# Performance work log

Hardware: AMD Instinct MI355X
Metric: run time of the kernel (lower is better)

Reference implementation:

```python
import jax, jax.numpy as jnp
import numpy as np

B, N, F_IN, F_E = 8, 64, 32, 16   # batch, nodes, node feat, edge feat
H = 64    # hidden_state_size
M = 64    # message_size
EH = 50   # edge_hidden_dim
T = 12    # l_target
RD = 200  # readout hidden_dim
NL = 3    # n_layers (message passing iterations, weight-tied)


def setup_inputs() -> dict:
    key = jax.random.key(0)
    ks = jax.random.split(key, 16)
    s = 0.05
    return {
        "g": jax.random.uniform(ks[0], (B, N, N), dtype=jnp.float32),
        "h_in": jax.random.uniform(ks[1], (B, N, F_IN), dtype=jnp.float32),
        "e": jax.random.normal(ks[2], (B, N, N, F_E), dtype=jnp.float32),
        # edge network MLP: edge_feat -> EH -> M*H
        "We1": jax.random.normal(ks[3], (F_E, EH)) * s,
        "be1": jnp.zeros((EH,)),
        "We2": jax.random.normal(ks[4], (EH, M * H)) * s,
        "be2": jnp.zeros((M * H,)),
        # GRU update (input = message M, hidden = H); gate order r, z, n
        "W_ih": jax.random.normal(ks[5], (3 * H, M)) * s,
        "W_hh": jax.random.normal(ks[6], (3 * H, H)) * s,
        "b_ih": jnp.zeros((3 * H,)),
        "b_hh": jnp.zeros((3 * H,)),
        # readout i-net: [h_T, h_0] (2H) -> RD -> T ; j-net: h_T (H) -> RD -> T
        "Wi1": jax.random.normal(ks[7], (2 * H, RD)) * s,
        "bi1": jnp.zeros((RD,)),
        "Wi2": jax.random.normal(ks[8], (RD, T)) * s,
        "bi2": jnp.zeros((T,)),
        "Wj1": jax.random.normal(ks[9], (H, RD)) * s,
        "bj1": jnp.zeros((RD,)),
        "Wj2": jax.random.normal(ks[10], (RD, T)) * s,
        "bj2": jnp.zeros((T,)),
    }


def reference(g, h_in, e, We1, be1, We2, be2, W_ih, W_hh, b_ih, b_hh,
              Wi1, bi1, Wi2, bi2, Wj1, bj1, Wj2, bj2):
    dt = h_in.dtype
    # pad node features with zeros up to hidden_state_size H
    h0 = jnp.concatenate(
        [h_in, jnp.zeros(h_in.shape[:2] + (H - F_IN,), dt)], axis=-1)  # (B,N,H)
    node_valid = (jnp.sum(h_in, axis=2) > 0).astype(dt)  # (B,N) mask applied each layer

    # edge network: per-edge (M,H) matrix A(e_vw); depends only on e, so compute once
    A = jnp.maximum(e @ We1 + be1, 0.0) @ We2 + be2        # (B,N,N,M*H)
    A = A.reshape(B, N, N, M, H)

    h = h0
    for _ in range(NL):
        # m[b,j] = sum_i g[b,i,j] * A(e[b,i,j]) @ h[b,i]
        # (original materializes m as (B,N,N,M), multiplies by g, sums over dim 1)
        m = jnp.einsum('bij,bijmh,bih->bjm', g, A, h)       # (B,N,M)
        # GRU cell update (PyTorch gate order: r, z, n)
        gi = m @ W_ih.T + b_ih                              # (B,N,3H)
        gh = h @ W_hh.T + b_hh
        r = jax.nn.sigmoid(gi[..., :H] + gh[..., :H])
        z = jax.nn.sigmoid(gi[..., H:2 * H] + gh[..., H:2 * H])
        n = jnp.tanh(gi[..., 2 * H:] + r * gh[..., 2 * H:])
        h = (1.0 - z) * n + z * h
        # zero out padding nodes: (sum(h_in,2) > 0) * h_t
        h = node_valid[..., None] * h

    # readout: R = sum_v mask_v * sigmoid(i([h_v^T, h_v^0])) * j(h_v^T)
    cat = jnp.concatenate([h, h0], axis=-1)                 # (B,N,2H)
    i_act = jax.nn.sigmoid(jnp.maximum(cat @ Wi1 + bi1, 0.0) @ Wi2 + bi2)
    j_act = jnp.maximum(h @ Wj1 + bj1, 0.0) @ Wj2 + bj2
    res = jnp.sum(node_valid[..., None] * i_act * j_act, axis=1)  # (B,T)
    return res
```

## Files before the change

### kernel.cpp

```cpp
#include <hip/hip_runtime.h>
#include <math.h>

#define BB 8
#define NN 64
#define F_IN 32
#define F_E 16
#define HH 64
#define MM 64
#define EHD 50
#define TT 12
#define RD 200
#define NL 3

#define KP 52
#define WROWS (KP * MM)
#define RLEN (NN * KP)
#define NODES (BB * NN)
#define IG 32

#define OFF_WAUG  0
#define SZ_WAUG   (WROWS * HH)
#define OFF_H0    (OFF_WAUG + SZ_WAUG)
#define OFF_H     (OFF_H0 + NODES * HH)
#define OFF_VALID (OFF_H + NODES * HH)
#define OFF_UG    (OFF_VALID + NODES)
#define SZ_UG     (BB * NN * RLEN)
#define OFF_C     (OFF_UG + SZ_UG)
#define SZ_C      (NODES * WROWS)
#define OFF_MPART (OFF_C + SZ_C)
#define SZ_MPART  (BB * IG * NN * MM)

__global__ __launch_bounds__(256) void prep_kernel(const float* __restrict__ h_in,
                                                   const float* __restrict__ We2,
                                                   const float* __restrict__ be2,
                                                   float* __restrict__ ws,
                                                   float* __restrict__ out) {
    int idx = blockIdx.x * 256 + threadIdx.x;
    float* Waug  = ws + OFF_WAUG;
    float* h0    = ws + OFF_H0;
    float* h     = ws + OFF_H;
    float* valid = ws + OFF_VALID;
    if (idx < SZ_WAUG) {
        int km = idx >> 6;
        int hv = idx & 63;
        int k  = km >> 6;
        int m  = km & 63;
        float v = 0.0f;
        if (k < EHD)       v = We2[k * (MM * HH) + m * HH + hv];
        else if (k == EHD) v = be2[m * HH + hv];
        Waug[idx] = v;
    } else if (idx < SZ_WAUG + NODES * HH) {
        int t = idx - SZ_WAUG;
        int n = t >> 6;
        int hv = t & 63;
        float v = (hv < F_IN) ? h_in[n * F_IN + hv] : 0.0f;
        h0[t] = v;
        h[t]  = v;
    } else if (idx < SZ_WAUG + NODES * HH + NODES) {
        int n = idx - SZ_WAUG - NODES * HH;
        float s = 0.0f;
        for (int c = 0; c < F_IN; ++c) s += h_in[n * F_IN + c];
        valid[n] = (s > 0.0f) ? 1.0f : 0.0f;
    } else if (idx < SZ_WAUG + NODES * HH + NODES + BB * TT) {
        out[idx - (SZ_WAUG + NODES * HH + NODES)] = 0.0f;
    }
}

__global__ __launch_bounds__(256) void edge_kernel(const float* __restrict__ g,
                                                   const float* __restrict__ e,
                                                   const float* __restrict__ We1,
                                                   const float* __restrict__ be1,
                                                   float* __restrict__ ws) {
    __shared__ float w1[F_E * EHD];
    __shared__ float b1[EHD];
    for (int t = threadIdx.x; t < F_E * EHD; t += 256) w1[t] = We1[t];
    if (threadIdx.x < EHD) b1[threadIdx.x] = be1[threadIdx.x];
    __syncthreads();

    int idx = blockIdx.x * 256 + threadIdx.x;
    int i = idx & 63;
    int j = (idx >> 6) & 63;
    int b = idx >> 12;

    const float* ep = e + ((size_t)((b * NN + i) * NN + j)) * F_E;
    float ev[F_E];
#pragma unroll
    for (int c = 0; c < F_E; c += 4) {
        float4 v = *(const float4*)(ep + c);
        ev[c] = v.x; ev[c + 1] = v.y; ev[c + 2] = v.z; ev[c + 3] = v.w;
    }
    float gv = g[(b * NN + i) * NN + j];

    float acc[EHD];
#pragma unroll
    for (int k = 0; k < EHD; ++k) acc[k] = b1[k];
#pragma unroll
    for (int c = 0; c < F_E; ++c) {
        float evc = ev[c];
#pragma unroll
        for (int k = 0; k < EHD; ++k) acc[k] += evc * w1[c * EHD + k];
    }
    float* ugp = ws + OFF_UG + ((size_t)(b * NN + j) * NN + i) * KP;
#pragma unroll
    for (int k = 0; k < EHD; ++k) ugp[k] = gv * fmaxf(acc[k], 0.0f);
    ugp[EHD]     = gv;
    ugp[EHD + 1] = 0.0f;
}

#define CG_BM 32
#define CG_BN 128
__global__ __launch_bounds__(256) void cgemm_kernel(float* __restrict__ ws) {
    const float* h    = ws + OFF_H;
    const float* Waug = ws + OFF_WAUG;
    float* C          = ws + OFF_C;

    __shared__ float hs[CG_BM * HH];
    __shared__ float wsh[CG_BN * HH];

    int tid = threadIdx.x;
    int kt = blockIdx.x;
    int nt = blockIdx.y;

    {
        const float4* src = (const float4*)(h + nt * CG_BM * HH);
        float4* dst = (float4*)hs;
#pragma unroll
        for (int q = 0; q < 2; ++q) dst[tid + q * 256] = src[tid + q * 256];
    }
    {
        const float4* src = (const float4*)(Waug + (size_t)kt * CG_BN * HH);
        float4* dst = (float4*)wsh;
#pragma unroll
        for (int q = 0; q < 8; ++q) {
            int fi = tid + q * 256;
            int row = fi >> 4, slot = fi & 15;
            dst[(row << 4) | (slot ^ (row & 15))] = src[fi];
        }
    }
    __syncthreads();

    int cg = tid & 31;
    int rg = tid >> 5;
    float acc[4][4];
#pragma unroll
    for (int q = 0; q < 4; ++q)
#pragma unroll
        for (int p = 0; p < 4; ++p) acc[q][p] = 0.0f;

#pragma unroll
    for (int hv = 0; hv < HH; hv += 4) {
        int slot = hv >> 2;
        float4 a[4], w[4];
#pragma unroll
        for (int q = 0; q < 4; ++q)
            a[q] = *(const float4*)(hs + (rg * 4 + q) * HH + hv);
#pragma unroll
        for (int p = 0; p < 4; ++p) {
            int row = cg + 32 * p;
            w[p] = ((const float4*)wsh)[(row << 4) | (slot ^ (row & 15))];
        }
#pragma unroll
        for (int q = 0; q < 4; ++q)
#pragma unroll
            for (int p = 0; p < 4; ++p)
                acc[q][p] += a[q].x * w[p].x + a[q].y * w[p].y +
                             a[q].z * w[p].z + a[q].w * w[p].w;
    }

#pragma unroll
    for (int q = 0; q < 4; ++q) {
        int node = nt * CG_BM + rg * 4 + q;
#pragma unroll
        for (int p = 0; p < 4; ++p) {
            int km = kt * CG_BN + cg + 32 * p;
            C[(size_t)node * WROWS + km] = acc[q][p];
        }
    }
}

__global__ __launch_bounds__(256) void msg_tiled_kernel(float* __restrict__ ws) {
    int blk = blockIdx.x;
    int b   = blk >> 5;
    int ig  = blk & 31;
    int i0  = ig * 2;

    const float* Cg  = ws + OFF_C  + (size_t)(b * NN + i0) * WROWS;
    const float* ugg = ws + OFF_UG + (size_t)(b * NN) * RLEN + i0 * KP;
    float* mp = ws + OFF_MPART + (size_t)(b * IG + ig) * (NN * MM);

    __shared__ float ug_t[104][64];
    __shared__ float C_s[104 * 64];

    int tid = threadIdx.x;
    {
        const float4* src = (const float4*)Cg;
        float4* dst = (float4*)C_s;
        for (int f = tid; f < 1664; f += 256) dst[f] = src[f];
    }
    {
        for (int f = tid; f < 1664; f += 256) {
            int j = f / 26, kq = f - j * 26;
            float4 v = *(const float4*)(ugg + (size_t)j * RLEN + kq * 4);
            ug_t[kq * 4 + 0][j] = v.x;
            ug_t[kq * 4 + 1][j] = v.y;
            ug_t[kq * 4 + 2][j] = v.z;
            ug_t[kq * 4 + 3][j] = v.w;
        }
    }
    __syncthreads();

    int tx = tid & 15;
    int ty = tid >> 4;
    float acc[4][4];
#pragma unroll
    for (int q = 0; q < 4; ++q)
#pragma unroll
        for (int p = 0; p < 4; ++p) acc[q][p] = 0.0f;

    const float4* C4 = (const float4*)C_s;
#pragma unroll 4
    for (int k = 0; k < 104; ++k) {
        float4 bv = C4[k * 16 + tx];
        float4 av = *(const float4*)(&ug_t[k][ty * 4]);
        acc[0][0] += av.x * bv.x; acc[0][1] += av.x * bv.y; acc[0][2] += av.x * bv.z; acc[0][3] += av.x * bv.w;
        acc[1][0] += av.y * bv.x; acc[1][1] += av.y * bv.y; acc[1][2] += av.y * bv.z; acc[1][3] += av.y * bv.w;
        acc[2][0] += av.z * bv.x; acc[2][1] += av.z * bv.y; acc[2][2] += av.z * bv.z; acc[2][3] += av.z * bv.w;
        acc[3][0] += av.w * bv.x; acc[3][1] += av.w * bv.y; acc[3][2] += av.w * bv.z; acc[3][3] += av.w * bv.w;
    }

#pragma unroll
    for (int q = 0; q < 4; ++q) {
        float4 o; o.x = acc[q][0]; o.y = acc[q][1]; o.z = acc[q][2]; o.w = acc[q][3];
        *(float4*)(mp + (size_t)(ty * 4 + q) * MM + tx * 4) = o;
    }
}

__global__ __launch_bounds__(256) void gru_reduce_kernel(const float* __restrict__ W_ih,
                                                         const float* __restrict__ W_hh,
                                                         const float* __restrict__ b_ih,
                                                         const float* __restrict__ b_hh,
                                                         float* __restrict__ ws) {
    int bj = blockIdx.x;
    int b = bj >> 6;
    int j = bj & 63;

    const float* mpart_g = ws + OFF_MPART;
    float* h           = ws + OFF_H;
    const float* valid = ws + OFF_VALID;

    __shared__ float mpart[4][MM];
    __shared__ float mv[MM];
    __shared__ float hv[HH];
    __shared__ float gi_s[3 * HH], gh_s[3 * HH];

    int lane = threadIdx.x & 63;
    int w    = threadIdx.x >> 6;

    if (threadIdx.x < HH) hv[threadIdx.x] = h[(size_t)bj * HH + threadIdx.x];

    float s = 0.0f;
#pragma unroll
    for (int q = 0; q < 8; ++q) {
        int ig = w * 8 + q;
        s += mpart_g[((size_t)(b * IG + ig) * NN + j) * MM + lane];
    }
    mpart[w][lane] = s;
    __syncthreads();

    if (threadIdx.x < MM)
        mv[threadIdx.x] = mpart[0][threadIdx.x] + mpart[1][threadIdx.x] +
                          mpart[2][threadIdx.x] + mpart[3][threadIdx.x];
    __syncthreads();

    if (threadIdx.x < 3 * HH) {
        int x = threadIdx.x;
        float gi = b_ih[x], gh = b_hh[x];
        const float4* wi = (const float4*)(W_ih + x * MM);
        const float4* wh = (const float4*)(W_hh + x * HH);
#pragma unroll
        for (int c = 0; c < HH / 4; ++c) {
            float4 aw = wi[c], bw = wh[c];
            gi += aw.x * mv[c * 4] + aw.y * mv[c * 4 + 1] + aw.z * mv[c * 4 + 2] + aw.w * mv[c * 4 + 3];
            gh += bw.x * hv[c * 4] + bw.y * hv[c * 4 + 1] + bw.z * hv[c * 4 + 2] + bw.w * hv[c * 4 + 3];
        }
        gi_s[x] = gi;
        gh_s[x] = gh;
    }
    __syncthreads();

    if (threadIdx.x < HH) {
        int t = threadIdx.x;
        float r = 1.0f / (1.0f + expf(-(gi_s[t] + gh_s[t])));
        float z = 1.0f / (1.0f + expf(-(gi_s[HH + t] + gh_s[HH + t])));
        float n = tanhf(gi_s[2 * HH + t] + r * gh_s[2 * HH + t]);
        float hn = (1.0f - z) * n + z * hv[t];
        h[(size_t)bj * HH + t] = hn * valid[bj];
    }
}

__global__ __launch_bounds__(64) void readout_kernel(const float* __restrict__ Wi1,
                                                     const float* __restrict__ bi1,
                                                     const float* __restrict__ Wi2,
                                                     const float* __restrict__ bi2,
                                                     const float* __restrict__ Wj1,
                                                     const float* __restrict__ bj1,
                                                     const float* __restrict__ Wj2,
                                                     const float* __restrict__ bj2,
                                                     float* __restrict__ ws,
                                                     float* __restrict__ out) {
    int node = blockIdx.x;
    int b = node >> 6;
    int t = threadIdx.x;

    __shared__ float cat[2 * HH];
    __shared__ float ih[RD], jh[RD];

    const float* h  = ws + OFF_H;
    const float* h0 = ws + OFF_H0;
    const float* valid = ws + OFF_VALID;

    cat[t]      = h[(size_t)node * HH + t];
    cat[64 + t] = h0[(size_t)node * HH + t];
    __syncthreads();

    bool has3 = (t + 192 < RD);
    int u3 = has3 ? (t + 192) : 0;
    float a0 = bi1[t], a1 = bi1[t + 64], a2 = bi1[t + 128], a3 = has3 ? bi1[u3] : 0.f;
    for (int c = 0; c < 2 * HH; ++c) {
        float cv = cat[c];
        const float* wr = Wi1 + c * RD;
        a0 += cv * wr[t];
        a1 += cv * wr[t + 64];
        a2 += cv * wr[t + 128];
        a3 += cv * wr[u3];
    }
    ih[t] = fmaxf(a0, 0.f); ih[t + 64] = fmaxf(a1, 0.f); ih[t + 128] = fmaxf(a2, 0.f);
    if (has3) ih[u3] = fmaxf(a3, 0.f);

    float c0 = bj1[t], c1 = bj1[t + 64], c2 = bj1[t + 128], c3 = has3 ? bj1[u3] : 0.f;
    for (int c = 0; c < HH; ++c) {
        float hvv = cat[c];
        const float* wr = Wj1 + c * RD;
        c0 += hvv * wr[t];
        c1 += hvv * wr[t + 64];
        c2 += hvv * wr[t + 128];
        c3 += hvv * wr[u3];
    }
    jh[t] = fmaxf(c0, 0.f); jh[t + 64] = fmaxf(c1, 0.f); jh[t + 128] = fmaxf(c2, 0.f);
    if (has3) jh[u3] = fmaxf(c3, 0.f);
    __syncthreads();

    if (t < TT) {
        float i2 = bi2[t], j2 = bj2[t];
        for (int u = 0; u < RD; ++u) {
            i2 += ih[u] * Wi2[u * TT + t];
            j2 += jh[u] * Wj2[u * TT + t];
        }
        float sig = 1.0f / (1.0f + expf(-i2));
        float contrib = valid[node] * sig * j2;
        atomicAdd(&out[b * TT + t], contrib);
    }
}

extern "C" void kernel_launch(void* const* d_in, const int* in_sizes, int n_in,
                              void* d_out, int out_size, void* d_ws, size_t ws_size,
                              hipStream_t stream) {
    (void)in_sizes; (void)n_in; (void)out_size; (void)ws_size;
    const float* g    = (const float*)d_in[0];
    const float* h_in = (const float*)d_in[1];
    const float* e    = (const float*)d_in[2];
    const float* We1  = (const float*)d_in[3];
    const float* be1  = (const float*)d_in[4];
    const float* We2  = (const float*)d_in[5];
    const float* be2  = (const float*)d_in[6];
    const float* W_ih = (const float*)d_in[7];
    const float* W_hh = (const float*)d_in[8];
    const float* b_ih = (const float*)d_in[9];
    const float* b_hh = (const float*)d_in[10];
    const float* Wi1  = (const float*)d_in[11];
    const float* bi1  = (const float*)d_in[12];
    const float* Wi2  = (const float*)d_in[13];
    const float* bi2  = (const float*)d_in[14];
    const float* Wj1  = (const float*)d_in[15];
    const float* bj1  = (const float*)d_in[16];
    const float* Wj2  = (const float*)d_in[17];
    const float* bj2  = (const float*)d_in[18];
    float* out = (float*)d_out;
    float* ws  = (float*)d_ws;

    const int prep_elems = SZ_WAUG + NODES * HH + NODES + BB * TT;
    prep_kernel<<<(prep_elems + 255) / 256, 256, 0, stream>>>(h_in, We2, be2, ws, out);
    edge_kernel<<<(BB * NN * NN) / 256, 256, 0, stream>>>(g, e, We1, be1, ws);

    for (int l = 0; l < NL; ++l) {
        cgemm_kernel<<<dim3(WROWS / CG_BN, NODES / CG_BM), 256, 0, stream>>>(ws);
        msg_tiled_kernel<<<BB * IG, 256, 0, stream>>>(ws);
        gru_reduce_kernel<<<NODES, 256, 0, stream>>>(W_ih, W_hh, b_ih, b_hh, ws);
    }

    readout_kernel<<<NODES, 64, 0, stream>>>(Wi1, bi1, Wi2, bi2, Wj1, bj1, Wj2, bj2, ws, out);
}
```

Measured before the change: 214.7 us.

## Fuse all stages into one cooperative persistent kernel with grid syncs

Replaces the eleven separate kernel launches (prep, edge, and cgemm/msg/gru per layer, readout) with a single cooperative kernel of 256 blocks that runs every stage and uses grid.sync between stages. The message kernel now stages one source node at a time to use less shared memory, and readout runs on 256-thread blocks. The goal is to remove per-launch overhead and tail gaps between the many small kernels. In exchange, grid-wide barriers add cost, fewer blocks cover the cgemm and GRU work, and the prep stage runs on only 128 blocks; a fallback multi-kernel path is kept in case the cooperative launch fails.

Measured after the change: 839.6 us. +291.0%, slower.

```diff
diff --git a/kernel.cpp b/kernel.cpp
--- a/kernel.cpp
+++ b/kernel.cpp
@@ -1,5 +1,8 @@
 #include <hip/hip_runtime.h>
+#include <hip/hip_cooperative_groups.h>
 #include <math.h>
+
+namespace cg = cooperative_groups;
 
 #define BB 8
 #define NN 64
@@ -18,69 +21,64 @@
 #define NODES (BB * NN)
 #define IG 32
 
+#define NTHR 256
+#define NBLK 256
+
 #define OFF_WAUG  0
 #define SZ_WAUG   (WROWS * HH)
 #define OFF_H0    (OFF_WAUG + SZ_WAUG)
 #define OFF_H     (OFF_H0 + NODES * HH)
 #define OFF_VALID (OFF_H + NODES * HH)
 #define OFF_UG    (OFF_VALID + NODES)
-#define SZ_UG     (BB * NN * RLEN)
+#define SZ_UG     (NODES * RLEN)
 #define OFF_C     (OFF_UG + SZ_UG)
 #define SZ_C      (NODES * WROWS)
 #define OFF_MPART (OFF_C + SZ_C)
 #define SZ_MPART  (BB * IG * NN * MM)
 
-__global__ __launch_bounds__(256) void prep_kernel(const float* __restrict__ h_in,
-                                                   const float* __restrict__ We2,
-                                                   const float* __restrict__ be2,
-                                                   float* __restrict__ ws,
-                                                   float* __restrict__ out) {
-    int idx = blockIdx.x * 256 + threadIdx.x;
+#define PREP_ELEMS (SZ_WAUG + NODES * HH + NODES + BB * TT)
+
+__device__ __forceinline__ void do_prep(int idx0, int stride,
+    const float* __restrict__ h_in, const float* __restrict__ We2,
+    const float* __restrict__ be2, float* __restrict__ ws, float* __restrict__ out)
+{
     float* Waug  = ws + OFF_WAUG;
     float* h0    = ws + OFF_H0;
     float* h     = ws + OFF_H;
     float* valid = ws + OFF_VALID;
-    if (idx < SZ_WAUG) {
-        int km = idx >> 6;
-        int hv = idx & 63;
-        int k  = km >> 6;
-        int m  = km & 63;
-        float v = 0.0f;
-        if (k < EHD)       v = We2[k * (MM * HH) + m * HH + hv];
-        else if (k == EHD) v = be2[m * HH + hv];
-        Waug[idx] = v;
-    } else if (idx < SZ_WAUG + NODES * HH) {
-        int t = idx - SZ_WAUG;
-        int n = t >> 6;
-        int hv = t & 63;
-        float v = (hv < F_IN) ? h_in[n * F_IN + hv] : 0.0f;
-        h0[t] = v;
-        h[t]  = v;
-    } else if (idx < SZ_WAUG + NODES * HH + NODES) {
-        int n = idx - SZ_WAUG - NODES * HH;
-        float s = 0.0f;
-        for (int c = 0; c < F_IN; ++c) s += h_in[n * F_IN + c];
-        valid[n] = (s > 0.0f) ? 1.0f : 0.0f;
-    } else if (idx < SZ_WAUG + NODES * HH + NODES + BB * TT) {
-        out[idx - (SZ_WAUG + NODES * HH + NODES)] = 0.0f;
-    }
-}
-
-__global__ __launch_bounds__(256) void edge_kernel(const float* __restrict__ g,
-                                                   const float* __restrict__ e,
-                                                   const float* __restrict__ We1,
-                                                   const float* __restrict__ be1,
-                                                   float* __restrict__ ws) {
-    __shared__ float w1[F_E * EHD];
-    __shared__ float b1[EHD];
-    for (int t = threadIdx.x; t < F_E * EHD; t += 256) w1[t] = We1[t];
-    if (threadIdx.x < EHD) b1[threadIdx.x] = be1[threadIdx.x];
-    __syncthreads();
-
-    int idx = blockIdx.x * 256 + threadIdx.x;
-    int i = idx & 63;
-    int j = (idx >> 6) & 63;
-    int b = idx >> 12;
+    for (int idx = idx0; idx < PREP_ELEMS; idx += stride) {
+        if (idx < SZ_WAUG) {
+            int km = idx >> 6, hv = idx & 63;
+            int k = km >> 6, m = km & 63;
+            float v = 0.0f;
+            if (k < EHD)       v = We2[k * (MM * HH) + m * HH + hv];
+            else if (k == EHD) v = be2[m * HH + hv];
+            Waug[idx] = v;
+        } else if (idx < SZ_WAUG + NODES * HH) {
+            int t = idx - SZ_WAUG;
+            int n = t >> 6, hv = t & 63;
+            float v = (hv < F_IN) ? h_in[n * F_IN + hv] : 0.0f;
+            h0[t] = v;
+            h[t]  = v;
+        } else if (idx < SZ_WAUG + NODES * HH + NODES) {
+            int n = idx - SZ_WAUG - NODES * HH;
+            float s = 0.0f;
+            for (int c = 0; c < F_IN; ++c) s += h_in[n * F_IN + c];
+            valid[n] = (s > 0.0f) ? 1.0f : 0.0f;
+        } else {
+            out[idx - (SZ_WAUG + NODES * HH + NODES)] = 0.0f;
+        }
+    }
+}
+
+__device__ __forceinline__ void do_edge(int eid,
+    const float* __restrict__ g, const float* __restrict__ e,
+    const float* __restrict__ w1, const float* __restrict__ b1,
+    float* __restrict__ ws)
+{
+    int i = eid & 63;
+    int j = (eid >> 6) & 63;
+    int b = eid >> 12;
 
     const float* ep = e + ((size_t)((b * NN + i) * NN + j)) * F_E;
     float ev[F_E];
@@ -107,28 +105,23 @@
     ugp[EHD + 1] = 0.0f;
 }
 
-#define CG_BM 32
-#define CG_BN 128
-__global__ __launch_bounds__(256) void cgemm_kernel(float* __restrict__ ws) {
+__device__ __forceinline__ void do_cgemm_tile(int kt, int nt, int tid,
+    float* __restrict__ lds, float* __restrict__ ws)
+{
     const float* h    = ws + OFF_H;
     const float* Waug = ws + OFF_WAUG;
     float* C          = ws + OFF_C;
-
-    __shared__ float hs[CG_BM * HH];
-    __shared__ float wsh[CG_BN * HH];
-
-    int tid = threadIdx.x;
-    int kt = blockIdx.x;
-    int nt = blockIdx.y;
+    float* hs  = lds;
+    float* wsh = lds + 2048;
 
     {
-        const float4* src = (const float4*)(h + nt * CG_BM * HH);
+        const float4* src = (const float4*)(h + nt * 32 * HH);
         float4* dst = (float4*)hs;
 #pragma unroll
         for (int q = 0; q < 2; ++q) dst[tid + q * 256] = src[tid + q * 256];
     }
     {
-        const float4* src = (const float4*)(Waug + (size_t)kt * CG_BN * HH);
+        const float4* src = (const float4*)(Waug + (size_t)kt * 128 * HH);
         float4* dst = (float4*)wsh;
 #pragma unroll
         for (int q = 0; q < 8; ++q) {
@@ -139,8 +132,8 @@
     }
     __syncthreads();
 
-    int cg = tid & 31;
-    int rg = tid >> 5;
+    int cgl = tid & 31;
+    int rg  = tid >> 5;
     float acc[4][4];
 #pragma unroll
     for (int q = 0; q < 4; ++q)
@@ -156,7 +149,7 @@
             a[q] = *(const float4*)(hs + (rg * 4 + q) * HH + hv);
 #pragma unroll
         for (int p = 0; p < 4; ++p) {
-            int row = cg + 32 * p;
+            int row = cgl + 32 * p;
             w[p] = ((const float4*)wsh)[(row << 4) | (slot ^ (row & 15))];
         }
 #pragma unroll
@@ -166,48 +159,24 @@
                 acc[q][p] += a[q].x * w[p].x + a[q].y * w[p].y +
                              a[q].z * w[p].z + a[q].w * w[p].w;
     }
+    __syncthreads();
 
 #pragma unroll
     for (int q = 0; q < 4; ++q) {
-        int node = nt * CG_BM + rg * 4 + q;
+        int node = nt * 32 + rg * 4 + q;
 #pragma unroll
         for (int p = 0; p < 4; ++p) {
-            int km = kt * CG_BN + cg + 32 * p;
+            int km = kt * 128 + cgl + 32 * p;
             C[(size_t)node * WROWS + km] = acc[q][p];
         }
     }
 }
 
-__global__ __launch_bounds__(256) void msg_tiled_kernel(float* __restrict__ ws) {
-    int blk = blockIdx.x;
-    int b   = blk >> 5;
-    int ig  = blk & 31;
-    int i0  = ig * 2;
-
-    const float* Cg  = ws + OFF_C  + (size_t)(b * NN + i0) * WROWS;
-    const float* ugg = ws + OFF_UG + (size_t)(b * NN) * RLEN + i0 * KP;
-    float* mp = ws + OFF_MPART + (size_t)(b * IG + ig) * (NN * MM);
-
-    __shared__ float ug_t[104][64];
-    __shared__ float C_s[104 * 64];
-
-    int tid = threadIdx.x;
-    {
-        const float4* src = (const float4*)Cg;
-        float4* dst = (float4*)C_s;
-        for (int f = tid; f < 1664; f += 256) dst[f] = src[f];
-    }
-    {
-        for (int f = tid; f < 1664; f += 256) {
-            int j = f / 26, kq = f - j * 26;
-            float4 v = *(const float4*)(ugg + (size_t)j * RLEN + kq * 4);
-            ug_t[kq * 4 + 0][j] = v.x;
-            ug_t[kq * 4 + 1][j] = v.y;
-            ug_t[kq * 4 + 2][j] = v.z;
-            ug_t[kq * 4 + 3][j] = v.w;
-        }
-    }
-    __syncthreads();
+__device__ __forceinline__ void do_msg_pair(int b, int ig, int tid,
+    float* __restrict__ lds, float* __restrict__ ws)
+{
+    float* C_s  = lds;
+    float* ug_t = lds + 3328;
 
     int tx = tid & 15;
     int ty = tid >> 4;
@@ -217,17 +186,39 @@
 #pragma unroll
         for (int p = 0; p < 4; ++p) acc[q][p] = 0.0f;
 
-    const float4* C4 = (const float4*)C_s;
+    for (int ii = 0; ii < 2; ++ii) {
+        int i = ig * 2 + ii;
+        const float* Cg  = ws + OFF_C  + (size_t)(b * NN + i) * WROWS;
+        const float* ugg = ws + OFF_UG + (size_t)(b * NN) * RLEN + i * KP;
+        {
+            const float4* src = (const float4*)Cg;
+            float4* dst = (float4*)C_s;
+            for (int f = tid; f < 832; f += NTHR) dst[f] = src[f];
+        }
+        for (int f = tid; f < 832; f += NTHR) {
+            int j = f / 13, kq = f - j * 13;
+            float4 v = *(const float4*)(ugg + (size_t)j * RLEN + kq * 4);
+            ug_t[(kq * 4 + 0) * 64 + j] = v.x;
+            ug_t[(kq * 4 + 1) * 64 + j] = v.y;
+            ug_t[(kq * 4 + 2) * 64 + j] = v.z;
+            ug_t[(kq * 4 + 3) * 64 + j] = v.w;
+        }
+        __syncthreads();
+
+        const float4* C4 = (const float4*)C_s;
 #pragma unroll 4
-    for (int k = 0; k < 104; ++k) {
-        float4 bv = C4[k * 16 + tx];
-        float4 av = *(const float4*)(&ug_t[k][ty * 4]);
-        acc[0][0] += av.x * bv.x; acc[0][1] += av.x * bv.y; acc[0][2] += av.x * bv.z; acc[0][3] += av.x * bv.w;
-        acc[1][0] += av.y * bv.x; acc[1][1] += av.y * bv.y; acc[1][2] += av.y * bv.z; acc[1][3] += av.y * bv.w;
-        acc[2][0] += av.z * bv.x; acc[2][1] += av.z * bv.y; acc[2][2] += av.z * bv.z; acc[2][3] += av.z * bv.w;
-        acc[3][0] += av.w * bv.x; acc[3][1] += av.w * bv.y; acc[3][2] += av.w * bv.z; acc[3][3] += av.w * bv.w;
-    }
-
+        for (int k = 0; k < KP; ++k) {
+            float4 bv = C4[k * 16 + tx];
+            float4 av = *(const float4*)(ug_t + k * 64 + ty * 4);
+            acc[0][0] += av.x * bv.x; acc[0][1] += av.x * bv.y; acc[0][2] += av.x * bv.z; acc[0][3] += av.x * bv.w;
+            acc[1][0] += av.y * bv.x; acc[1][1] += av.y * bv.y; acc[1][2] += av.y * bv.z; acc[1][3] += av.y * bv.w;
+            acc[2][0] += av.z * bv.x; acc[2][1] += av.z * bv.y; acc[2][2] += av.z * bv.z; acc[2][3] += av.z * bv.w;
+            acc[3][0] += av.w * bv.x; acc[3][1] += av.w * bv.y; acc[3][2] += av.w * bv.z; acc[3][3] += av.w * bv.w;
+        }
+        __syncthreads();
+    }
+
+    float* mp = ws + OFF_MPART + (size_t)(b * IG + ig) * (NN * MM);
 #pragma unroll
     for (int q = 0; q < 4; ++q) {
         float4 o; o.x = acc[q][0]; o.y = acc[q][1]; o.z = acc[q][2]; o.w = acc[q][3];
@@ -235,45 +226,38 @@
     }
 }
 
-__global__ __launch_bounds__(256) void gru_reduce_kernel(const float* __restrict__ W_ih,
-                                                         const float* __restrict__ W_hh,
-                                                         const float* __restrict__ b_ih,
-                                                         const float* __restrict__ b_hh,
-                                                         float* __restrict__ ws) {
-    int bj = blockIdx.x;
-    int b = bj >> 6;
-    int j = bj & 63;
-
-    const float* mpart_g = ws + OFF_MPART;
+__device__ __forceinline__ void do_gru(int node, int tid,
+    float* __restrict__ lds, float* __restrict__ ws,
+    const float* __restrict__ W_ih, const float* __restrict__ W_hh,
+    const float* __restrict__ b_ih, const float* __restrict__ b_hh)
+{
+    int b = node >> 6, j = node & 63;
+    float* mpart = lds;
+    float* mv    = lds + 256;
+    float* hvs   = lds + 320;
+    float* gi_s  = lds + 384;
+    float* gh_s  = lds + 576;
     float* h           = ws + OFF_H;
     const float* valid = ws + OFF_VALID;
 
-    __shared__ float mpart[4][MM];
-    __shared__ float mv[MM];
-    __shared__ float hv[HH];
-    __shared__ float gi_s[3 * HH], gh_s[3 * HH];
-
-    int lane = threadIdx.x & 63;
-    int w    = threadIdx.x >> 6;
-
-    if (threadIdx.x < HH) hv[threadIdx.x] = h[(size_t)bj * HH + threadIdx.x];
+    int lane = tid & 63, w = tid >> 6;
+    if (tid < HH) hvs[tid] = h[(size_t)node * HH + tid];
 
     float s = 0.0f;
 #pragma unroll
     for (int q = 0; q < 8; ++q) {
         int ig = w * 8 + q;
-        s += mpart_g[((size_t)(b * IG + ig) * NN + j) * MM + lane];
-    }
-    mpart[w][lane] = s;
-    __syncthreads();
-
-    if (threadIdx.x < MM)
-        mv[threadIdx.x] = mpart[0][threadIdx.x] + mpart[1][threadIdx.x] +
-                          mpart[2][threadIdx.x] + mpart[3][threadIdx.x];
-    __syncthreads();
-
-    if (threadIdx.x < 3 * HH) {
-        int x = threadIdx.x;
+        s += ws[OFF_MPART + ((size_t)(b * IG + ig) * NN + j) * MM + lane];
+    }
+    mpart[w * 64 + lane] = s;
+    __syncthreads();
+
+    if (tid < MM)
+        mv[tid] = mpart[tid] + mpart[64 + tid] + mpart[128 + tid] + mpart[192 + tid];
+    __syncthreads();
+
+    if (tid < 3 * HH) {
+        int x = tid;
         float gi = b_ih[x], gh = b_hh[x];
         const float4* wi = (const float4*)(W_ih + x * MM);
         const float4* wh = (const float4*)(W_hh + x * HH);
@@ -281,85 +265,164 @@
         for (int c = 0; c < HH / 4; ++c) {
             float4 aw = wi[c], bw = wh[c];
             gi += aw.x * mv[c * 4] + aw.y * mv[c * 4 + 1] + aw.z * mv[c * 4 + 2] + aw.w * mv[c * 4 + 3];
-            gh += bw.x * hv[c * 4] + bw.y * hv[c * 4 + 1] + bw.z * hv[c * 4 + 2] + bw.w * hv[c * 4 + 3];
+            gh += bw.x * hvs[c * 4] + bw.y * hvs[c * 4 + 1] + bw.z * hvs[c * 4 + 2] + bw.w * hvs[c * 4 + 3];
         }
         gi_s[x] = gi;
         gh_s[x] = gh;
     }
     __syncthreads();
 
-    if (threadIdx.x < HH) {
-        int t = threadIdx.x;
-        float r = 1.0f / (1.0f + expf(-(gi_s[t] + gh_s[t])));
-        float z = 1.0f / (1.0f + expf(-(gi_s[HH + t] + gh_s[HH + t])));
-        float n = tanhf(gi_s[2 * HH + t] + r * gh_s[2 * HH + t]);
-        float hn = (1.0f - z) * n + z * hv[t];
-        h[(size_t)bj * HH + t] = hn * valid[bj];
-    }
-}
-
-__global__ __launch_bounds__(64) void readout_kernel(const float* __restrict__ Wi1,
-                                                     const float* __restrict__ bi1,
-                                                     const float* __restrict__ Wi2,
-                                                     const float* __restrict__ bi2,
-                                                     const float* __restrict__ Wj1,
-                                                     const float* __restrict__ bj1,
-                                                     const float* __restrict__ Wj2,
-                                                     const float* __restrict__ bj2,
-                                                     float* __restrict__ ws,
-                                                     float* __restrict__ out) {
-    int node = blockIdx.x;
+    if (tid < HH) {
+        float r = 1.0f / (1.0f + expf(-(gi_s[tid] + gh_s[tid])));
+        float z = 1.0f / (1.0f + expf(-(gi_s[HH + tid] + gh_s[HH + tid])));
+        float n = tanhf(gi_s[2 * HH + tid] + r * gh_s[2 * HH + tid]);
+        float hn = (1.0f - z) * n + z * hvs[tid];
+        h[(size_t)node * HH + tid] = hn * valid[node];
+    }
+    __syncthreads();
+}
+
+__device__ __forceinline__ void do_readout(int node, int tid,
+    float* __restrict__ lds, float* __restrict__ ws,
+    const float* __restrict__ Wi1, const float* __restrict__ bi1,
+    const float* __restrict__ Wi2, const float* __restrict__ bi2,
+    const float* __restrict__ Wj1, const float* __restrict__ bj1,
+    const float* __restrict__ Wj2, const float* __restrict__ bj2,
+    float* __restrict__ out)
+{
+    float* cat = lds;
+    float* ih  = lds + 128;
+    float* jh  = lds + 328;
+    const float* h     = ws + OFF_H;
+    const float* h0    = ws + OFF_H0;
+    const float* valid = ws + OFF_VALID;
     int b = node >> 6;
-    int t = threadIdx.x;
-
-    __shared__ float cat[2 * HH];
-    __shared__ float ih[RD], jh[RD];
-
-    const float* h  = ws + OFF_H;
-    const float* h0 = ws + OFF_H0;
-    const float* valid = ws + OFF_VALID;
-
-    cat[t]      = h[(size_t)node * HH + t];
-    cat[64 + t] = h0[(size_t)node * HH + t];
-    __syncthreads();
-
-    bool has3 = (t + 192 < RD);
-    int u3 = has3 ? (t + 192) : 0;
-    float a0 = bi1[t], a1 = bi1[t + 64], a2 = bi1[t + 128], a3 = has3 ? bi1[u3] : 0.f;
-    for (int c = 0; c < 2 * HH; ++c) {
-        float cv = cat[c];
-        const float* wr = Wi1 + c * RD;
-        a0 += cv * wr[t];
-        a1 += cv * wr[t + 64];
-        a2 += cv * wr[t + 128];
-        a3 += cv * wr[u3];
-    }
-    ih[t] = fmaxf(a0, 0.f); ih[t + 64] = fmaxf(a1, 0.f); ih[t + 128] = fmaxf(a2, 0.f);
-    if (has3) ih[u3] = fmaxf(a3, 0.f);
-
-    float c0 = bj1[t], c1 = bj1[t + 64], c2 = bj1[t + 128], c3 = has3 ? bj1[u3] : 0.f;
-    for (int c = 0; c < HH; ++c) {
-        float hvv = cat[c];
-        const float* wr = Wj1 + c * RD;
-        c0 += hvv * wr[t];
-        c1 += hvv * wr[t + 64];
-        c2 += hvv * wr[t + 128];
-        c3 += hvv * wr[u3];
-    }
-    jh[t] = fmaxf(c0, 0.f); jh[t + 64] = fmaxf(c1, 0.f); jh[t + 128] = fmaxf(c2, 0.f);
-    if (has3) jh[u3] = fmaxf(c3, 0.f);
-    __syncthreads();
-
-    if (t < TT) {
-        float i2 = bi2[t], j2 = bj2[t];
+
+    if (tid < 2 * HH)
+        cat[tid] = (tid < HH) ? h[(size_t)node * HH + tid]
+                              : h0[(size_t)node * HH + (tid - HH)];
+    __syncthreads();
+
+    if (tid < RD) {
+        float a = bi1[tid];
+        for (int c = 0; c < 2 * HH; ++c) a += cat[c] * Wi1[c * RD + tid];
+        ih[tid] = fmaxf(a, 0.0f);
+        float bj = bj1[tid];
+        for (int c = 0; c < HH; ++c) bj += cat[c] * Wj1[c * RD + tid];
+        jh[tid] = fmaxf(bj, 0.0f);
+    }
+    __syncthreads();
+
+    if (tid < TT) {
+        float i2 = bi2[tid], j2 = bj2[tid];
         for (int u = 0; u < RD; ++u) {
-            i2 += ih[u] * Wi2[u * TT + t];
-            j2 += jh[u] * Wj2[u * TT + t];
+            i2 += ih[u] * Wi2[u * TT + tid];
+            j2 += jh[u] * Wj2[u * TT + tid];
         }
         float sig = 1.0f / (1.0f + expf(-i2));
-        float contrib = valid[node] * sig * j2;
-        atomicAdd(&out[b * TT + t], contrib);
-    }
+        atomicAdd(&out[b * TT + tid], valid[node] * sig * j2);
+    }
+    __syncthreads();
+}
+
+__global__ __launch_bounds__(NTHR) void mega_kernel(
+    const float* __restrict__ g,   const float* __restrict__ h_in,
+    const float* __restrict__ e,
+    const float* __restrict__ We1, const float* __restrict__ be1,
+    const float* __restrict__ We2, const float* __restrict__ be2,
+    const float* __restrict__ W_ih, const float* __restrict__ W_hh,
+    const float* __restrict__ b_ih, const float* __restrict__ b_hh,
+    const float* __restrict__ Wi1, const float* __restrict__ bi1,
+    const float* __restrict__ Wi2, const float* __restrict__ bi2,
+    const float* __restrict__ Wj1, const float* __restrict__ bj1,
+    const float* __restrict__ Wj2, const float* __restrict__ bj2,
+    float* __restrict__ ws, float* __restrict__ out)
+{
+    cg::grid_group grid = cg::this_grid();
+    __shared__ float lds[10240];
+
+    const int blk = blockIdx.x;
+    const int tid = threadIdx.x;
+
+    if (blk < 128) {
+        do_prep(blk * NTHR + tid, 128 * NTHR, h_in, We2, be2, ws, out);
+    } else {
+        float* w1 = lds;
+        float* b1 = lds + F_E * EHD;
+        for (int t = tid; t < F_E * EHD; t += NTHR) w1[t] = We1[t];
+        if (tid < EHD) b1[tid] = be1[tid];
+        __syncthreads();
+        do_edge((blk - 128) * NTHR + tid, g, e, w1, b1, ws);
+    }
+    __threadfence(); grid.sync();
+
+    for (int l = 0; l < NL; ++l) {
+        for (int t = blk; t < 416; t += NBLK)
+            do_cgemm_tile(t % 26, t / 26, tid, lds, ws);
+        __threadfence(); grid.sync();
+
+        do_msg_pair(blk >> 5, blk & 31, tid, lds, ws);
+        __threadfence(); grid.sync();
+
+        for (int n = blk; n < NODES; n += NBLK)
+            do_gru(n, tid, lds, ws, W_ih, W_hh, b_ih, b_hh);
+        __threadfence(); grid.sync();
+    }
+
+    for (int n = blk; n < NODES; n += NBLK)
+        do_readout(n, tid, lds, ws, Wi1, bi1, Wi2, bi2, Wj1, bj1, Wj2, bj2, out);
+}
+
+__global__ __launch_bounds__(NTHR) void k_prep(const float* __restrict__ h_in,
+    const float* __restrict__ We2, const float* __restrict__ be2,
+    float* __restrict__ ws, float* __restrict__ out)
+{
+    do_prep(blockIdx.x * NTHR + threadIdx.x, gridDim.x * NTHR, h_in, We2, be2, ws, out);
+}
+
+__global__ __launch_bounds__(NTHR) void k_edge(const float* __restrict__ g,
+    const float* __restrict__ e, const float* __restrict__ We1,
+    const float* __restrict__ be1, float* __restrict__ ws)
+{
+    __shared__ float lds[F_E * EHD + EHD];
+    float* w1 = lds;
+    float* b1 = lds + F_E * EHD;
+    for (int t = threadIdx.x; t < F_E * EHD; t += NTHR) w1[t] = We1[t];
+    if (threadIdx.x < EHD) b1[threadIdx.x] = be1[threadIdx.x];
+    __syncthreads();
+    do_edge(blockIdx.x * NTHR + threadIdx.x, g, e, w1, b1, ws);
+}
+
+__global__ __launch_bounds__(NTHR) void k_cgemm(float* __restrict__ ws)
+{
+    __shared__ float lds[10240];
+    do_cgemm_tile(blockIdx.x % 26, blockIdx.x / 26, threadIdx.x, lds, ws);
+}
+
+__global__ __launch_bounds__(NTHR) void k_msg(float* __restrict__ ws)
+{
+    __shared__ float lds[6656];
+    do_msg_pair(blockIdx.x >> 5, blockIdx.x & 31, threadIdx.x, lds, ws);
+}
+
+__global__ __launch_bounds__(NTHR) void k_gru(const float* __restrict__ W_ih,
+    const float* __restrict__ W_hh, const float* __restrict__ b_ih,
+    const float* __restrict__ b_hh, float* __restrict__ ws)
+{
+    __shared__ float lds[768];
+    do_gru(blockIdx.x, threadIdx.x, lds, ws, W_ih, W_hh, b_ih, b_hh);
+}
+
+__global__ __launch_bounds__(NTHR) void k_readout(
+    const float* __restrict__ Wi1, const float* __restrict__ bi1,
+    const float* __restrict__ Wi2, const float* __restrict__ bi2,
+    const float* __restrict__ Wj1, const float* __restrict__ bj1,
+    const float* __restrict__ Wj2, const float* __restrict__ bj2,
+    float* __restrict__ ws, float* __restrict__ out)
+{
+    __shared__ float lds[528];
+    do_readout(blockIdx.x, threadIdx.x, lds, ws,
+               Wi1, bi1, Wi2, bi2, Wj1, bj1, Wj2, bj2, out);
 }
 
 extern "C" void kernel_launch(void* const* d_in, const int* in_sizes, int n_in,
@@ -388,15 +451,25 @@
     float* out = (float*)d_out;
     float* ws  = (float*)d_ws;
 
-    const int prep_elems = SZ_WAUG + NODES * HH + NODES + BB * TT;
-    prep_kernel<<<(prep_elems + 255) / 256, 256, 0, stream>>>(h_in, We2, be2, ws, out);
-    edge_kernel<<<(BB * NN * NN) / 256, 256, 0, stream>>>(g, e, We1, be1, ws);
-
-    for (int l = 0; l < NL; ++l) {
-        cgemm_kernel<<<dim3(WROWS / CG_BN, NODES / CG_BM), 256, 0, stream>>>(ws);
-        msg_tiled_kernel<<<BB * IG, 256, 0, stream>>>(ws);
-        gru_reduce_kernel<<<NODES, 256, 0, stream>>>(W_ih, W_hh, b_ih, b_hh, ws);
-    }
-
-    readout_kernel<<<NODES, 64, 0, stream>>>(Wi1, bi1, Wi2, bi2, Wj1, bj1, Wj2, bj2, ws, out);
-}
+    void* args[] = {
+        (void*)&g, (void*)&h_in, (void*)&e,
+        (void*)&We1, (void*)&be1, (void*)&We2, (void*)&be2,
+        (void*)&W_ih, (void*)&W_hh, (void*)&b_ih, (void*)&b_hh,
+        (void*)&Wi1, (void*)&bi1, (void*)&Wi2, (void*)&bi2,
+        (void*)&Wj1, (void*)&bj1, (void*)&Wj2, (void*)&bj2,
+        (void*)&ws, (void*)&out
+    };
+    hipError_t err = hipLaunchCooperativeKernel((void*)mega_kernel, dim3(NBLK),
+                                                dim3(NTHR), args, 0, stream);
+    if (err != hipSuccess) {
+        k_prep<<<(PREP_ELEMS + NTHR - 1) / NTHR, NTHR, 0, stream>>>(h_in, We2, be2, ws, out);
+        k_edge<<<(BB * NN * NN) / NTHR, NTHR, 0, stream>>>(g, e, We1, be1, ws);
+        for (int l = 0; l < NL; ++l) {
+            k_cgemm<<<416, NTHR, 0, stream>>>(ws);
+            k_msg<<<256, NTHR, 0, stream>>>(ws);
+            k_gru<<<NODES, NTHR, 0, stream>>>(W_ih, W_hh, b_ih, b_hh, ws);
+        }
+        k_readout<<<NODES, NTHR, 0, stream>>>(Wi1, bi1, Wi2, bi2,
+                                              Wj1, bj1, Wj2, bj2, ws, out);
+    }
+}
```
